# Performance work log

Hardware: AMD Instinct MI355X
Metric: run time of the kernel (lower is better)

Reference implementation:

```python
import jax, jax.numpy as jnp
import numpy as np

B, N, C, H = 8, 1024, 768, 12
D = C // H  # head_dim = 64
SCALE = D ** -0.5


def setup_inputs() -> dict:
    key = jax.random.key(0)
    k1, k2, k3, k4 = jax.random.split(key, 4)
    x = jax.random.normal(k1, (B, N, C), dtype=jnp.float32)
    spe_agg = jax.random.normal(k2, (B, C), dtype=jnp.float32)
    # nn.Linear(dim, dim*3, bias=False): weight shape (3C, C), y = x @ W.T
    W_qkv = jax.random.normal(k3, (3 * C, C), dtype=jnp.float32) * (C ** -0.5)
    W_proj = jax.random.normal(k4, (C, C), dtype=jnp.float32) * (C ** -0.5)
    b_proj = jnp.zeros((C,), dtype=jnp.float32)
    return {"x": x, "spe_agg": spe_agg, "W_qkv": W_qkv, "W_proj": W_proj, "b_proj": b_proj}


def reference(x, spe_agg, W_qkv, W_proj, b_proj):
    b, n, c = x.shape
    qkv = x @ W_qkv.T  # (B, N, 3C)
    q = qkv[..., :c].reshape(b, n, H, D).transpose(0, 2, 1, 3)        # (B,H,N,D)
    k = qkv[..., c:2 * c].reshape(b, n, H, D).transpose(0, 2, 1, 3)   # (B,H,N,D)
    # v projection from qkv is discarded in the original module;
    # v = ones(B,N,C) * spe_agg[:,None,:] broadcast over N
    v = jnp.broadcast_to(spe_agg[:, None, :], (b, n, c)).reshape(b, n, H, D).transpose(0, 2, 1, 3)
    attn = jax.nn.softmax(jnp.einsum('bhnd,bhmd->bhnm', q, k) * SCALE, axis=-1)
    out = jnp.einsum('bhnm,bhmd->bhnd', attn, v)                      # (B,H,N,D)
    out = out.transpose(0, 2, 1, 3).reshape(b, n, c)                  # (B,N,C)
    return out @ W_proj.T + b_proj
```

## Files before the change

### kernel.cpp

```cpp
#include <hip/hip_runtime.h>

#define BB 8
#define NN 1024
#define CC 768

__global__ __launch_bounds__(256) void proj_gemv_kernel(
    const float* __restrict__ spe,
    const float* __restrict__ Wp,
    const float* __restrict__ bp,
    float* __restrict__ r)
{
    const int wave = (blockIdx.x * blockDim.x + threadIdx.x) >> 6;
    const int lane = threadIdx.x & 63;
    const int b = wave / CC;
    const int c = wave - b * CC;

    const float* wrow = Wp + (size_t)c * CC;
    const float* srow = spe + (size_t)b * CC;

    float acc = 0.0f;
#pragma unroll
    for (int j = 0; j < 3; ++j) {
        const int base = (j * 64 + lane) * 4;
        float4 w4 = *reinterpret_cast<const float4*>(wrow + base);
        float4 s4 = *reinterpret_cast<const float4*>(srow + base);
        acc = fmaf(w4.x, s4.x, acc);
        acc = fmaf(w4.y, s4.y, acc);
        acc = fmaf(w4.z, s4.z, acc);
        acc = fmaf(w4.w, s4.w, acc);
    }
#pragma unroll
    for (int off = 32; off > 0; off >>= 1)
        acc += __shfl_down(acc, off, 64);

    if (lane == 0) {
        r[b * CC + c] = acc + bp[c];
    }
}

__global__ __launch_bounds__(256) void bcast_kernel(
    const float4* __restrict__ r,
    float4* __restrict__ out)
{
    const int i = blockIdx.x * blockDim.x + threadIdx.x;
    const int row = i / (CC / 4);
    const int c4  = i - row * (CC / 4);
    const int b   = row >> 10;
    out[i] = r[b * (CC / 4) + c4];
}

extern "C" void kernel_launch(void* const* d_in, const int* in_sizes, int n_in,
                              void* d_out, int out_size, void* d_ws, size_t ws_size,
                              hipStream_t stream) {
    const float* spe = (const float*)d_in[1];
    const float* Wp  = (const float*)d_in[3];
    const float* bp  = (const float*)d_in[4];
    float* r = (float*)d_ws;

    proj_gemv_kernel<<<dim3((BB * CC) / 4), dim3(256), 0, stream>>>(spe, Wp, bp, r);

    bcast_kernel<<<dim3((BB * NN * CC / 4) / 256), dim3(256), 0, stream>>>(
        (const float4*)r, (float4*)d_out);
}
```

Measured before the change: 87.39 us.

## Fuse projection GEMV and row broadcast into a single kernel

Merges the GEMV that projects spe_agg through W_proj with the kernel that broadcasts the result over all N rows. Each block computes 64 output columns for one batch into shared memory, then writes them to a 128-row slab of the output. This removes a second launch and the workspace round-trip. In exchange, every row group recomputes the same GEMV columns, and stores become 256-byte row segments instead of fully contiguous rows.

Measured after the change: 94.79 us. 1.08x slower.

```diff
diff --git a/kernel.cpp b/kernel.cpp
--- a/kernel.cpp
+++ b/kernel.cpp
@@ -3,50 +3,64 @@
 #define BB 8
 #define NN 1024
 #define CC 768
+#define COLS 64
+#define RG 8
+#define ROWS (NN / RG)
 
-__global__ __launch_bounds__(256) void proj_gemv_kernel(
+__global__ __launch_bounds__(256) void fused_proj_bcast_kernel(
     const float* __restrict__ spe,
     const float* __restrict__ Wp,
     const float* __restrict__ bp,
-    float* __restrict__ r)
+    float* __restrict__ out)
 {
-    const int wave = (blockIdx.x * blockDim.x + threadIdx.x) >> 6;
-    const int lane = threadIdx.x & 63;
-    const int b = wave / CC;
-    const int c = wave - b * CC;
+    __shared__ float rs[COLS];
 
-    const float* wrow = Wp + (size_t)c * CC;
+    const int blk = blockIdx.x;
+    const int rg  = blk & (RG - 1);
+    const int t2  = blk >> 3;
+    const int ct  = t2 % (CC / COLS);
+    const int b   = t2 / (CC / COLS);
+
+    const int tid  = threadIdx.x;
+    const int wave = tid >> 6;
+    const int lane = tid & 63;
+
     const float* srow = spe + (size_t)b * CC;
 
-    float acc = 0.0f;
+    for (int i = 0; i < 16; ++i) {
+        const int col = ct * COLS + wave * 16 + i;
+        const float* wrow = Wp + (size_t)col * CC;
+        float acc = 0.0f;
 #pragma unroll
-    for (int j = 0; j < 3; ++j) {
-        const int base = (j * 64 + lane) * 4;
-        float4 w4 = *reinterpret_cast<const float4*>(wrow + base);
-        float4 s4 = *reinterpret_cast<const float4*>(srow + base);
-        acc = fmaf(w4.x, s4.x, acc);
-        acc = fmaf(w4.y, s4.y, acc);
-        acc = fmaf(w4.z, s4.z, acc);
-        acc = fmaf(w4.w, s4.w, acc);
+        for (int j = 0; j < 3; ++j) {
+            const int base = (j * 64 + lane) * 4;
+            float4 w4 = *reinterpret_cast<const float4*>(wrow + base);
+            float4 s4 = *reinterpret_cast<const float4*>(srow + base);
+            acc = fmaf(w4.x, s4.x, acc);
+            acc = fmaf(w4.y, s4.y, acc);
+            acc = fmaf(w4.z, s4.z, acc);
+            acc = fmaf(w4.w, s4.w, acc);
+        }
+#pragma unroll
+        for (int off = 32; off > 0; off >>= 1)
+            acc += __shfl_down(acc, off, 64);
+        if (lane == 0)
+            rs[wave * 16 + i] = acc + bp[col];
     }
+    __syncthreads();
+
+    const float4* rsv = reinterpret_cast<const float4*>(rs);
+    const int c4 = tid & 15;
+    const int r0 = tid >> 4;
+    const float4 val = rsv[c4];
+
+    float4* outp = reinterpret_cast<float4*>(out) + (size_t)b * NN * (CC / 4);
+    const int row_base = rg * ROWS;
 #pragma unroll
-    for (int off = 32; off > 0; off >>= 1)
-        acc += __shfl_down(acc, off, 64);
-
-    if (lane == 0) {
-        r[b * CC + c] = acc + bp[c];
+    for (int it = 0; it < ROWS / 16; ++it) {
+        const int row = row_base + it * 16 + r0;
+        outp[(size_t)row * (CC / 4) + ct * 16 + c4] = val;
     }
-}
-
-__global__ __launch_bounds__(256) void bcast_kernel(
-    const float4* __restrict__ r,
-    float4* __restrict__ out)
-{
-    const int i = blockIdx.x * blockDim.x + threadIdx.x;
-    const int row = i / (CC / 4);
-    const int c4  = i - row * (CC / 4);
-    const int b   = row >> 10;
-    out[i] = r[b * (CC / 4) + c4];
 }
 
 extern "C" void kernel_launch(void* const* d_in, const int* in_sizes, int n_in,
@@ -55,10 +69,8 @@
     const float* spe = (const float*)d_in[1];
     const float* Wp  = (const float*)d_in[3];
     const float* bp  = (const float*)d_in[4];
-    float* r = (float*)d_ws;
+    float* out = (float*)d_out;
 
-    proj_gemv_kernel<<<dim3((BB * CC) / 4), dim3(256), 0, stream>>>(spe, Wp, bp, r);
-
-    bcast_kernel<<<dim3((BB * NN * CC / 4) / 256), dim3(256), 0, stream>>>(
-        (const float4*)r, (float4*)d_out);
+    fused_proj_bcast_kernel<<<dim3(BB * (CC / COLS) * RG), dim3(256), 0, stream>>>(
+        spe, Wp, bp, out);
 }
```
